# Kernel tuning notes

Hardware: AMD Instinct MI355X
Metric: run time of the kernel (lower is better)

The kernel has to match this reference:

```python
import jax, jax.numpy as jnp
import numpy as np

EMBED_DIM = 768
NUM_HEADS = 12
HEAD_SIZE = EMBED_DIM // NUM_HEADS


def setup_inputs() -> dict:
    key = jax.random.key(0)
    ks = jax.random.split(key, 9)
    B, S, D = 4, 2048, EMBED_DIM
    scale = 1.0 / np.sqrt(D)
    x = jax.random.normal(ks[0], (B, S, D), dtype=jnp.float32)
    # Linear params (torch nn.Linear: y = x @ W.T + b); store W as [in, out] for einsum
    Wq = jax.random.normal(ks[1], (D, D), dtype=jnp.float32) * scale
    bq = jnp.zeros((D,), dtype=jnp.float32)
    Wk = jax.random.normal(ks[2], (D, D), dtype=jnp.float32) * scale
    bk = jnp.zeros((D,), dtype=jnp.float32)
    Wv = jax.random.normal(ks[3], (D, D), dtype=jnp.float32) * scale
    bv = jnp.zeros((D,), dtype=jnp.float32)
    Wo = jax.random.normal(ks[4], (D, D), dtype=jnp.float32) * scale
    bo = jnp.zeros((D,), dtype=jnp.float32)
    return {"x": x, "Wq": Wq, "bq": bq, "Wk": Wk, "bk": bk,
            "Wv": Wv, "bv": bv, "Wo": Wo, "bo": bo}


def reference(x, Wq, bq, Wk, bk, Wv, bv, Wo, bo):
    B, S, D = x.shape
    H, hs = NUM_HEADS, HEAD_SIZE
    scale = hs ** (-0.5)
    # Projections
    Q = (x @ Wq + bq).reshape(B, S, H, hs)
    K = (x @ Wk + bk).reshape(B, S, H, hs)
    V = (x @ Wv + bv).reshape(B, S, H, hs)
    # Batched attention over all heads (equivalent to the per-head loop:
    # torch view splits last dim into H contiguous chunks; concat of per-head
    # outputs along -1 restores the same layout)
    scores = jnp.einsum('bqhd,bkhd->bhqk', Q, K) * scale  # [B,H,S,S]
    attn = jax.nn.softmax(scores, axis=-1)
    out = jnp.einsum('bhqk,bkhd->bqhd', attn, V).reshape(B, S, D)
    # Output projection; dropout is identity in eval mode
    return out @ Wo + bo
```

## Files before the change

kernel.cpp:

```cpp
#include <hip/hip_runtime.h>

typedef unsigned short ushort_t;
typedef __bf16 bf16x8 __attribute__((ext_vector_type(8)));
typedef float floatx4 __attribute__((ext_vector_type(4)));

__device__ inline ushort_t f2bf(float f) {
    __bf16 h = (__bf16)f;
    return __builtin_bit_cast(ushort_t, h);
}

__device__ inline void gload16(const void* g, void* l) {
    __builtin_amdgcn_global_load_lds((const __attribute__((address_space(1))) void*)g,
                                     (__attribute__((address_space(3))) void*)l, 16, 0, 0);
}

__global__ __launch_bounds__(256) void prep_kernel(
    const float* __restrict__ x, ushort_t* __restrict__ xbf,
    const float* __restrict__ W0, const float* __restrict__ W1,
    const float* __restrict__ W2, const float* __restrict__ W3,
    ushort_t* __restrict__ T0, ushort_t* __restrict__ T1,
    ushort_t* __restrict__ T2, ushort_t* __restrict__ T3) {
    int bx = blockIdx.x;
    int tid = threadIdx.x;
    if (bx < 2304) {
        __shared__ float t[32][33];
        int w = bx / 576, rem = bx % 576;
        const float* W; ushort_t* T;
        switch (w) {
            case 0: W = W0; T = T0; break;
            case 1: W = W1; T = T1; break;
            case 2: W = W2; T = T2; break;
            default: W = W3; T = T3; break;
        }
        int n0 = (rem / 24) * 32, k0 = (rem % 24) * 32;
        int tx = tid & 31, ty = tid >> 5;
        for (int i = 0; i < 4; ++i)
            t[ty + i * 8][tx] = W[(k0 + ty + i * 8) * 768 + n0 + tx];
        __syncthreads();
        for (int i = 0; i < 4; ++i)
            T[(n0 + ty + i * 8) * 768 + k0 + tx] = f2bf(t[tx][ty + i * 8]);
    } else {
        int i = ((bx - 2304) * 256 + tid) * 4;
        float4 v = *(const float4*)(x + i);
        ushort4 u;
        u.x = f2bf(v.x); u.y = f2bf(v.y); u.z = f2bf(v.z); u.w = f2bf(v.w);
        *(ushort4*)(xbf + i) = u;
    }
}

__global__ __launch_bounds__(256) void gemm_qkv(
    const ushort_t* __restrict__ A,
    const ushort_t* __restrict__ Tq, const ushort_t* __restrict__ Tk, const ushort_t* __restrict__ Tv,
    const float* __restrict__ bq, const float* __restrict__ bk, const float* __restrict__ bv,
    ushort_t* __restrict__ Qb, ushort_t* __restrict__ Kb, ushort_t* __restrict__ Vtb) {
    __shared__ ushort_t sh[128 * 64 + 64 * 64];
    ushort_t* As = sh;
    ushort_t* Bs = sh + 128 * 64;
    int tid = threadIdx.x;
    int m0 = blockIdx.x * 128;
    int by = blockIdx.y;
    int which = by / 12;
    int n0 = (by % 12) * 64;
    const ushort_t* Bt = which == 0 ? Tq : (which == 1 ? Tk : Tv);
    const float* bias = which == 0 ? bq : (which == 1 ? bk : bv);

    int wave = tid >> 6;
    int lane = tid & 63;
    int ln = tid & 15;
    int quad = (tid >> 4) & 3;
    int wm = wave * 32;
    int lr = lane >> 3;
    int lc = (lane & 7) * 8;

    floatx4 acc[2][4];
    floatx4 z = {0.f, 0.f, 0.f, 0.f};
    for (int i = 0; i < 2; ++i)
        for (int j = 0; j < 4; ++j) acc[i][j] = z;

    for (int kt = 0; kt < 12; ++kt) {
        int k0 = kt * 64;
        __syncthreads();
        for (int i = 0; i < 4; ++i) {
            int c = wave * 4 + i;
            gload16(&A[(m0 + c * 8 + lr) * 768 + k0 + lc], &As[c * 512]);
        }
        for (int i = 0; i < 2; ++i) {
            int c = wave * 2 + i;
            gload16(&Bt[(n0 + c * 8 + lr) * 768 + k0 + lc], &Bs[c * 512]);
        }
        __syncthreads();
        for (int ks = 0; ks < 2; ++ks) {
            bf16x8 a[2], b[4];
            for (int i = 0; i < 2; ++i)
                a[i] = *(const bf16x8*)&As[(wm + i * 16 + ln) * 64 + ks * 32 + quad * 8];
            for (int j = 0; j < 4; ++j)
                b[j] = *(const bf16x8*)&Bs[(j * 16 + ln) * 64 + ks * 32 + quad * 8];
            for (int i = 0; i < 2; ++i)
                for (int j = 0; j < 4; ++j)
                    acc[i][j] = __builtin_amdgcn_mfma_f32_16x16x32_bf16(a[i], b[j], acc[i][j], 0, 0, 0);
        }
    }

    const float QSCALE = 0.125f * 1.44269504088896f;
    if (which != 2) {
        for (int i = 0; i < 2; ++i) {
            for (int j = 0; j < 4; ++j) {
                int gn = n0 + j * 16 + ln;
                float bia = bias[gn];
                int h = gn >> 6, dd = gn & 63;
                for (int r = 0; r < 4; ++r) {
                    int gm = m0 + wm + i * 16 + quad * 4 + r;
                    int bb = gm >> 11, ss = gm & 2047;
                    float v = acc[i][j][r] + bia;
                    if (which == 0) {
                        Qb[((bb * 12 + h) * 2048 + ss) * 64 + dd] = f2bf(v * QSCALE);
                    } else {
                        Kb[((bb * 12 + h) * 2048 + ss) * 64 + dd] = f2bf(v);
                    }
                }
            }
        }
    } else {
        __syncthreads();
        ushort_t* tr = sh;
        for (int j = 0; j < 4; ++j) {
            int nl = j * 16 + ln;
            float bia = bias[n0 + nl];
            for (int i = 0; i < 2; ++i) {
                ushort4 u;
                u.x = f2bf(acc[i][j][0] + bia);
                u.y = f2bf(acc[i][j][1] + bia);
                u.z = f2bf(acc[i][j][2] + bia);
                u.w = f2bf(acc[i][j][3] + bia);
                *(ushort4*)&tr[nl * 136 + wm + i * 16 + quad * 4] = u;
            }
        }
        __syncthreads();
        int bb = m0 >> 11, ss0 = m0 & 2047;
        int head = by % 12;
        for (int p = 0; p < 4; ++p) {
            int n = p * 16 + (tid >> 4);
            int mc = (tid & 15) * 8;
            uint4 v = *(const uint4*)&tr[n * 136 + mc];
            *(uint4*)&Vtb[(size_t)((bb * 12 + head) * 64 + n) * 2048 + ss0 + mc] = v;
        }
    }
}

__global__ __launch_bounds__(256, 2) void attn_kernel(
    const ushort_t* __restrict__ Qb, const ushort_t* __restrict__ Kb,
    const ushort_t* __restrict__ Vtb, ushort_t* __restrict__ Ob) {
    __shared__ ushort_t Ks[2][64 * 72];
    __shared__ ushort_t Vs[2][64 * 72];
    int tid = threadIdx.x;
    int bid = blockIdx.x;
    int swz = (bid & 7) * 96 + (bid >> 3);
    int bh = swz >> 4;
    int qt = swz & 15;
    int wave = tid >> 6;
    int qh = wave >> 1;
    int kh = wave & 1;
    int ln = tid & 15;
    int quad = (tid >> 4) & 3;
    int q0 = qt * 128 + qh * 64;

    const ushort_t* Qp = Qb + (size_t)bh * 2048 * 64;
    const ushort_t* Kp = Kb + (size_t)bh * 2048 * 64;
    const ushort_t* Vp = Vtb + (size_t)bh * 64 * 2048;

    bf16x8 bqf[4][2];
    for (int g = 0; g < 4; ++g)
        for (int ks = 0; ks < 2; ++ks)
            bqf[g][ks] = *(const bf16x8*)&Qp[(q0 + g * 16 + ln) * 64 + ks * 32 + quad * 8];

    int srow = tid >> 3;
    int c8 = tid & 7;
    int scol = c8 * 8;
    int u = c8 & 3;
    int vcol = (c8 >> 2) * 32 + (u & 1) * 16 + (u >> 1) * 4;

    uint4 kreg[2], vreg[2];

    for (int p = 0; p < 2; ++p) {
        kreg[p] = *(const uint4*)&Kp[(p * 32 + srow) * 64 + scol];
        vreg[p] = *(const uint4*)&Vp[(p * 32 + srow) * 2048 + scol];
    }
    for (int p = 0; p < 2; ++p) {
        *(uint4*)&Ks[0][(p * 32 + srow) * 72 + scol] = kreg[p];
        ushort_t* vb = &Vs[0][(p * 32 + srow) * 72 + vcol];
        *(uint2*)vb = make_uint2(vreg[p].x, vreg[p].y);
        *(uint2*)(vb + 8) = make_uint2(vreg[p].z, vreg[p].w);
    }
    __syncthreads();

    floatx4 o_acc[4][4];
    float lsum[4] = {0.f, 0.f, 0.f, 0.f};
    floatx4 z = {0.f, 0.f, 0.f, 0.f};
    for (int g = 0; g < 4; ++g)
        for (int m4 = 0; m4 < 4; ++m4) o_acc[g][m4] = z;

    for (int kt = 0; kt < 32; ++kt) {
        int cur = kt & 1;
        if (kt < 31) {
            for (int p = 0; p < 2; ++p) {
                kreg[p] = *(const uint4*)&Kp[((kt + 1) * 64 + p * 32 + srow) * 64 + scol];
                vreg[p] = *(const uint4*)&Vp[(p * 32 + srow) * 2048 + (kt + 1) * 64 + scol];
            }
        }

        const ushort_t* KsH = Ks[cur];
        const ushort_t* VsH = Vs[cur];

        bf16x8 ak[2][2];
        for (int m = 0; m < 2; ++m)
            for (int ks = 0; ks < 2; ++ks)
                ak[m][ks] = *(const bf16x8*)&KsH[((kh * 2 + m) * 16 + ln) * 72 + ks * 32 + quad * 8];

        floatx4 st[4][2];
        for (int g = 0; g < 4; ++g)
            for (int m = 0; m < 2; ++m) {
                floatx4 s = z;
                s = __builtin_amdgcn_mfma_f32_16x16x32_bf16(ak[m][0], bqf[g][0], s, 0, 0, 0);
                s = __builtin_amdgcn_mfma_f32_16x16x32_bf16(ak[m][1], bqf[g][1], s, 0, 0, 0);
                st[g][m] = s;
            }

        for (int g = 0; g < 4; ++g)
            for (int m = 0; m < 2; ++m)
                for (int r = 0; r < 4; ++r) {
                    float e = __builtin_amdgcn_exp2f(st[g][m][r]);
                    st[g][m][r] = e;
                    lsum[g] += e;
                }

        bf16x8 av[4];
        for (int m4 = 0; m4 < 4; ++m4)
            av[m4] = *(const bf16x8*)&VsH[(m4 * 16 + ln) * 72 + kh * 32 + quad * 8];

        for (int g = 0; g < 4; ++g) {
            bf16x8 b;
            b[0] = (__bf16)st[g][0][0];
            b[1] = (__bf16)st[g][0][1];
            b[2] = (__bf16)st[g][0][2];
            b[3] = (__bf16)st[g][0][3];
            b[4] = (__bf16)st[g][1][0];
            b[5] = (__bf16)st[g][1][1];
            b[6] = (__bf16)st[g][1][2];
            b[7] = (__bf16)st[g][1][3];
            for (int m4 = 0; m4 < 4; ++m4)
                o_acc[g][m4] = __builtin_amdgcn_mfma_f32_16x16x32_bf16(av[m4], b, o_acc[g][m4], 0, 0, 0);
        }

        if (kt < 31) {
            int nxt = cur ^ 1;
            for (int p = 0; p < 2; ++p) {
                *(uint4*)&Ks[nxt][(p * 32 + srow) * 72 + scol] = kreg[p];
                ushort_t* vb = &Vs[nxt][(p * 32 + srow) * 72 + vcol];
                *(uint2*)vb = make_uint2(vreg[p].x, vreg[p].y);
                *(uint2*)(vb + 8) = make_uint2(vreg[p].z, vreg[p].w);
            }
        }
        __syncthreads();
    }

    for (int g = 0; g < 4; ++g) {
        lsum[g] += __shfl_xor(lsum[g], 16);
        lsum[g] += __shfl_xor(lsum[g], 32);
    }

    float* mbuf = (float*)&Ks[0][0];
    float* lbuf = mbuf + 2 * 64 * 68;
    if (kh == 1) {
        float* base = mbuf + qh * 64 * 68;
        for (int g = 0; g < 4; ++g) {
            for (int m4 = 0; m4 < 4; ++m4)
                *(floatx4*)&base[(g * 16 + ln) * 68 + m4 * 16 + quad * 4] = o_acc[g][m4];
            if (quad == 0) lbuf[qh * 64 + g * 16 + ln] = lsum[g];
        }
    }
    __syncthreads();

    int b = bh / 12, h = bh % 12;
    if (kh == 0) {
        float* base = mbuf + qh * 64 * 68;
        for (int g = 0; g < 4; ++g) {
            float inv = 1.f / (lsum[g] + lbuf[qh * 64 + g * 16 + ln]);
            int token = b * 2048 + q0 + g * 16 + ln;
            for (int m4 = 0; m4 < 4; ++m4) {
                floatx4 o2 = *(const floatx4*)&base[(g * 16 + ln) * 68 + m4 * 16 + quad * 4];
                for (int r = 0; r < 4; ++r)
                    Ob[token * 768 + h * 64 + m4 * 16 + quad * 4 + r] =
                        f2bf((o_acc[g][m4][r] + o2[r]) * inv);
            }
        }
    }
}

__global__ __launch_bounds__(256) void gemm_out(
    const ushort_t* __restrict__ A, const ushort_t* __restrict__ Bt,
    const float* __restrict__ bias, float* __restrict__ out) {
    __shared__ ushort_t As[128 * 64];
    __shared__ ushort_t Bs[64 * 64];
    int tid = threadIdx.x;
    int m0 = blockIdx.x * 128;
    int n0 = blockIdx.y * 64;

    int wave = tid >> 6;
    int lane = tid & 63;
    int ln = tid & 15;
    int quad = (tid >> 4) & 3;
    int wm = wave * 32;
    int lr = lane >> 3;
    int lc = (lane & 7) * 8;

    floatx4 acc[2][4];
    floatx4 z = {0.f, 0.f, 0.f, 0.f};
    for (int i = 0; i < 2; ++i)
        for (int j = 0; j < 4; ++j) acc[i][j] = z;

    for (int kt = 0; kt < 12; ++kt) {
        int k0 = kt * 64;
        __syncthreads();
        for (int i = 0; i < 4; ++i) {
            int c = wave * 4 + i;
            gload16(&A[(m0 + c * 8 + lr) * 768 + k0 + lc], &As[c * 512]);
        }
        for (int i = 0; i < 2; ++i) {
            int c = wave * 2 + i;
            gload16(&Bt[(n0 + c * 8 + lr) * 768 + k0 + lc], &Bs[c * 512]);
        }
        __syncthreads();
        for (int ks = 0; ks < 2; ++ks) {
            bf16x8 a[2], b[4];
            for (int i = 0; i < 2; ++i)
                a[i] = *(const bf16x8*)&As[(wm + i * 16 + ln) * 64 + ks * 32 + quad * 8];
            for (int j = 0; j < 4; ++j)
                b[j] = *(const bf16x8*)&Bs[(j * 16 + ln) * 64 + ks * 32 + quad * 8];
            for (int i = 0; i < 2; ++i)
                for (int j = 0; j < 4; ++j)
                    acc[i][j] = __builtin_amdgcn_mfma_f32_16x16x32_bf16(a[i], b[j], acc[i][j], 0, 0, 0);
        }
    }

    for (int i = 0; i < 2; ++i) {
        for (int j = 0; j < 4; ++j) {
            int gn = n0 + j * 16 + ln;
            float bia = bias[gn];
            for (int r = 0; r < 4; ++r) {
                int gm = m0 + wm + i * 16 + quad * 4 + r;
                out[gm * 768 + gn] = acc[i][j][r] + bia;
            }
        }
    }
}

extern "C" void kernel_launch(void* const* d_in, const int* in_sizes, int n_in,
                              void* d_out, int out_size, void* d_ws, size_t ws_size,
                              hipStream_t stream) {
    const float* x  = (const float*)d_in[0];
    const float* Wq = (const float*)d_in[1];
    const float* bq = (const float*)d_in[2];
    const float* Wk = (const float*)d_in[3];
    const float* bk = (const float*)d_in[4];
    const float* Wv = (const float*)d_in[5];
    const float* bv = (const float*)d_in[6];
    const float* Wo = (const float*)d_in[7];
    const float* bo = (const float*)d_in[8];

    const int NTOK = 4 * 2048;
    const int NELT = NTOK * 768;
    const int WELT = 768 * 768;

    ushort_t* xbf = (ushort_t*)d_ws;
    ushort_t* Tq  = xbf + NELT;
    ushort_t* Tk  = Tq + WELT;
    ushort_t* Tv  = Tk + WELT;
    ushort_t* To  = Tv + WELT;
    ushort_t* Qb  = To + WELT;
    ushort_t* Kb  = Qb + NELT;
    ushort_t* Vtb = Kb + NELT;
    ushort_t* Ob  = Vtb + NELT;

    prep_kernel<<<8448, 256, 0, stream>>>(x, xbf, Wq, Wk, Wv, Wo, Tq, Tk, Tv, To);
    gemm_qkv<<<dim3(64, 36), 256, 0, stream>>>(xbf, Tq, Tk, Tv, bq, bk, bv, Qb, Kb, Vtb);
    attn_kernel<<<768, 256, 0, stream>>>(Qb, Kb, Vtb, Ob);
    gemm_out<<<dim3(64, 12), 256, 0, stream>>>(Ob, To, bo, (float*)d_out);
}
```

Baseline: 216.3 us.

## Load K fragments directly to registers and remap QKV GEMM blocks per XCD

```diff
diff --git a/kernel.cpp b/kernel.cpp
--- a/kernel.cpp
+++ b/kernel.cpp
@@ -57,8 +57,12 @@
     ushort_t* As = sh;
     ushort_t* Bs = sh + 128 * 64;
     int tid = threadIdx.x;
-    int m0 = blockIdx.x * 128;
-    int by = blockIdx.y;
+    int bid = blockIdx.x;
+    int xcd = bid & 7;
+    int idx = bid >> 3;
+    int bx = xcd * 8 + (idx & 7);
+    int by = idx >> 3;
+    int m0 = bx * 128;
     int which = by / 12;
     int n0 = (by % 12) * 64;
     const ushort_t* Bt = which == 0 ? Tq : (which == 1 ? Tk : Tv);
@@ -150,7 +154,6 @@
 __global__ __launch_bounds__(256, 2) void attn_kernel(
     const ushort_t* __restrict__ Qb, const ushort_t* __restrict__ Kb,
     const ushort_t* __restrict__ Vtb, ushort_t* __restrict__ Ob) {
-    __shared__ ushort_t Ks[2][64 * 72];
     __shared__ ushort_t Vs[2][64 * 72];
     int tid = threadIdx.x;
     int bid = blockIdx.x;
@@ -179,18 +182,19 @@
     int u = c8 & 3;
     int vcol = (c8 >> 2) * 32 + (u & 1) * 16 + (u >> 1) * 4;
 
-    uint4 kreg[2], vreg[2];
-
+    uint4 vreg[2];
+
+    for (int p = 0; p < 2; ++p)
+        vreg[p] = *(const uint4*)&Vp[(p * 32 + srow) * 2048 + scol];
     for (int p = 0; p < 2; ++p) {
-        kreg[p] = *(const uint4*)&Kp[(p * 32 + srow) * 64 + scol];
-        vreg[p] = *(const uint4*)&Vp[(p * 32 + srow) * 2048 + scol];
-    }
-    for (int p = 0; p < 2; ++p) {
-        *(uint4*)&Ks[0][(p * 32 + srow) * 72 + scol] = kreg[p];
         ushort_t* vb = &Vs[0][(p * 32 + srow) * 72 + vcol];
         *(uint2*)vb = make_uint2(vreg[p].x, vreg[p].y);
         *(uint2*)(vb + 8) = make_uint2(vreg[p].z, vreg[p].w);
     }
+    bf16x8 akc[2][2];
+    for (int m = 0; m < 2; ++m)
+        for (int ks = 0; ks < 2; ++ks)
+            akc[m][ks] = *(const bf16x8*)&Kp[((kh * 2 + m) * 16 + ln) * 64 + ks * 32 + quad * 8];
     __syncthreads();
 
     floatx4 o_acc[4][4];
@@ -201,27 +205,23 @@
 
     for (int kt = 0; kt < 32; ++kt) {
         int cur = kt & 1;
+        bf16x8 akn[2][2];
         if (kt < 31) {
-            for (int p = 0; p < 2; ++p) {
-                kreg[p] = *(const uint4*)&Kp[((kt + 1) * 64 + p * 32 + srow) * 64 + scol];
+            for (int p = 0; p < 2; ++p)
                 vreg[p] = *(const uint4*)&Vp[(p * 32 + srow) * 2048 + (kt + 1) * 64 + scol];
-            }
-        }
-
-        const ushort_t* KsH = Ks[cur];
+            for (int m = 0; m < 2; ++m)
+                for (int ks = 0; ks < 2; ++ks)
+                    akn[m][ks] = *(const bf16x8*)&Kp[((kt + 1) * 64 + (kh * 2 + m) * 16 + ln) * 64 + ks * 32 + quad * 8];
+        }
+
         const ushort_t* VsH = Vs[cur];
-
-        bf16x8 ak[2][2];
-        for (int m = 0; m < 2; ++m)
-            for (int ks = 0; ks < 2; ++ks)
-                ak[m][ks] = *(const bf16x8*)&KsH[((kh * 2 + m) * 16 + ln) * 72 + ks * 32 + quad * 8];
 
         floatx4 st[4][2];
         for (int g = 0; g < 4; ++g)
             for (int m = 0; m < 2; ++m) {
                 floatx4 s = z;
-                s = __builtin_amdgcn_mfma_f32_16x16x32_bf16(ak[m][0], bqf[g][0], s, 0, 0, 0);
-                s = __builtin_amdgcn_mfma_f32_16x16x32_bf16(ak[m][1], bqf[g][1], s, 0, 0, 0);
+                s = __builtin_amdgcn_mfma_f32_16x16x32_bf16(akc[m][0], bqf[g][0], s, 0, 0, 0);
+                s = __builtin_amdgcn_mfma_f32_16x16x32_bf16(akc[m][1], bqf[g][1], s, 0, 0, 0);
                 st[g][m] = s;
             }
 
@@ -254,11 +254,13 @@
         if (kt < 31) {
             int nxt = cur ^ 1;
             for (int p = 0; p < 2; ++p) {
-                *(uint4*)&Ks[nxt][(p * 32 + srow) * 72 + scol] = kreg[p];
                 ushort_t* vb = &Vs[nxt][(p * 32 + srow) * 72 + vcol];
                 *(uint2*)vb = make_uint2(vreg[p].x, vreg[p].y);
                 *(uint2*)(vb + 8) = make_uint2(vreg[p].z, vreg[p].w);
             }
+            for (int m = 0; m < 2; ++m)
+                for (int ks = 0; ks < 2; ++ks)
+                    akc[m][ks] = akn[m][ks];
         }
         __syncthreads();
     }
@@ -268,31 +270,31 @@
         lsum[g] += __shfl_xor(lsum[g], 32);
     }
 
-    float* mbuf = (float*)&Ks[0][0];
-    float* lbuf = mbuf + 2 * 64 * 68;
-    if (kh == 1) {
-        float* base = mbuf + qh * 64 * 68;
-        for (int g = 0; g < 4; ++g) {
-            for (int m4 = 0; m4 < 4; ++m4)
-                *(floatx4*)&base[(g * 16 + ln) * 68 + m4 * 16 + quad * 4] = o_acc[g][m4];
-            if (quad == 0) lbuf[qh * 64 + g * 16 + ln] = lsum[g];
-        }
-    }
-    __syncthreads();
-
+    float* mbuf = (float*)&Vs[0][0];
+    float* lbuf = mbuf + 64 * 68;
     int b = bh / 12, h = bh % 12;
-    if (kh == 0) {
-        float* base = mbuf + qh * 64 * 68;
-        for (int g = 0; g < 4; ++g) {
-            float inv = 1.f / (lsum[g] + lbuf[qh * 64 + g * 16 + ln]);
-            int token = b * 2048 + q0 + g * 16 + ln;
-            for (int m4 = 0; m4 < 4; ++m4) {
-                floatx4 o2 = *(const floatx4*)&base[(g * 16 + ln) * 68 + m4 * 16 + quad * 4];
-                for (int r = 0; r < 4; ++r)
-                    Ob[token * 768 + h * 64 + m4 * 16 + quad * 4 + r] =
-                        f2bf((o_acc[g][m4][r] + o2[r]) * inv);
-            }
-        }
+    for (int ph = 0; ph < 2; ++ph) {
+        if (kh == 1 && qh == ph) {
+            for (int g = 0; g < 4; ++g) {
+                for (int m4 = 0; m4 < 4; ++m4)
+                    *(floatx4*)&mbuf[(g * 16 + ln) * 68 + m4 * 16 + quad * 4] = o_acc[g][m4];
+                if (quad == 0) lbuf[g * 16 + ln] = lsum[g];
+            }
+        }
+        __syncthreads();
+        if (kh == 0 && qh == ph) {
+            for (int g = 0; g < 4; ++g) {
+                float inv = 1.f / (lsum[g] + lbuf[g * 16 + ln]);
+                int token = b * 2048 + q0 + g * 16 + ln;
+                for (int m4 = 0; m4 < 4; ++m4) {
+                    floatx4 o2 = *(const floatx4*)&mbuf[(g * 16 + ln) * 68 + m4 * 16 + quad * 4];
+                    for (int r = 0; r < 4; ++r)
+                        Ob[token * 768 + h * 64 + m4 * 16 + quad * 4 + r] =
+                            f2bf((o_acc[g][m4][r] + o2[r]) * inv);
+                }
+            }
+        }
+        __syncthreads();
     }
 }
 
@@ -382,7 +384,7 @@
     ushort_t* Ob  = Vtb + NELT;
 
     prep_kernel<<<8448, 256, 0, stream>>>(x, xbf, Wq, Wk, Wv, Wo, Tq, Tk, Tv, To);
-    gemm_qkv<<<dim3(64, 36), 256, 0, stream>>>(xbf, Tq, Tk, Tv, bq, bk, bv, Qb, Kb, Vtb);
+    gemm_qkv<<<2304, 256, 0, stream>>>(xbf, Tq, Tk, Tv, bq, bk, bv, Qb, Kb, Vtb);
     attn_kernel<<<768, 256, 0, stream>>>(Qb, Kb, Vtb, Ob);
     gemm_out<<<dim3(64, 12), 256, 0, stream>>>(Ob, To, bo, (float*)d_out);
 }
```

Measured after the change: 239.7 us. +10.8%, slower.
